# Kernel tuning notes

Hardware: AMD Instinct MI355X
Metric: run time of the kernel (lower is better)

Reference implementation:

```python
import jax, jax.numpy as jnp
import numpy as np

N_NODES = 100000
N_EDGES = 1600000
N_GRAPHS = 512
IN_C, HID, OUT_C = 128, 128, 64


def gcn_conv(x, W, b, src, dst, num_nodes):
    # PyG GCNConv: add self-loops, symmetric normalization D^-1/2 (A+I) D^-1/2, then linear.
    h = x @ W  # [N, F_out]
    deg = jnp.ones((num_nodes,), h.dtype).at[dst].add(jnp.ones((src.shape[0],), h.dtype))  # +1 for self-loop
    dinv = jax.lax.rsqrt(deg)
    norm = dinv[src] * dinv[dst]  # [E]
    agg = jnp.zeros_like(h).at[dst].add(h[src] * norm[:, None])
    agg = agg + h * (dinv * dinv)[:, None]  # self-loop contribution
    return agg + b


def global_mean_pool(x, batch, num_graphs):
    s = jax.ops.segment_sum(x, batch, num_segments=num_graphs)
    cnt = jax.ops.segment_sum(jnp.ones((x.shape[0],), x.dtype), batch, num_segments=num_graphs)
    return s / jnp.maximum(cnt, 1.0)[:, None]


def setup_inputs() -> dict:
    key = jax.random.key(0)
    ks = jax.random.split(key, 16)
    glorot = lambda k, i, o: jax.random.normal(k, (i, o), jnp.float32) * (2.0 / (i + o)) ** 0.5
    inp = {
        "x": jax.random.normal(ks[0], (N_NODES, IN_C), jnp.float32),
        "edge_index": jax.random.randint(ks[1], (2, N_EDGES), 0, N_NODES, jnp.int64 if jax.config.jax_enable_x64 else jnp.int32),
        "batch": jnp.sort(jax.random.randint(ks[2], (N_NODES,), 0, N_GRAPHS)),
        "W1": glorot(ks[3], IN_C, HID), "b1": jnp.zeros((HID,), jnp.float32),
        "W2": glorot(ks[4], HID, HID), "b2": jnp.zeros((HID,), jnp.float32),
        "W3": glorot(ks[5], HID, HID), "b3": jnp.zeros((HID,), jnp.float32),
        "Wf1": glorot(ks[6], HID, HID * 4), "bf1": jnp.zeros((HID * 4,), jnp.float32),
        "Wf2": glorot(ks[7], HID * 4, HID * 2), "bf2": jnp.zeros((HID * 2,), jnp.float32),
        "Wf3": glorot(ks[8], HID * 2, HID), "bf3": jnp.zeros((HID,), jnp.float32),
        "Wf4": glorot(ks[9], HID, OUT_C), "bf4": jnp.zeros((OUT_C,), jnp.float32),
    }
    return inp


def reference(x, edge_index, batch, W1, b1, W2, b2, W3, b3,
              Wf1, bf1, Wf2, bf2, Wf3, bf3, Wf4, bf4):
    src, dst = edge_index[0], edge_index[1]
    h = jax.nn.relu(gcn_conv(x, W1, b1, src, dst, N_NODES))
    h = jax.nn.relu(gcn_conv(h, W2, b2, src, dst, N_NODES))
    h = gcn_conv(h, W3, b3, src, dst, N_NODES)
    f = global_mean_pool(h, batch, N_GRAPHS)  # [G, HID]
    z = jax.nn.relu(f @ Wf1 + bf1)
    z = jax.nn.relu(z @ Wf2 + bf2)
    z = jax.nn.relu(z @ Wf3 + bf3)
    z = z @ Wf4 + bf4
    return (f, z)
```

## Files before the change

kernel.cpp:

```cpp
#include <hip/hip_runtime.h>
#include <hip/hip_bf16.h>

#define NN 100000
#define NE 1600000
#define NG 512
#define HID 128
#define PPART 391
#define EPB 4096
#define CAP 4608

typedef __attribute__((ext_vector_type(8))) short short8;
typedef __attribute__((ext_vector_type(4))) float floatx4;

__device__ inline ushort f2bf(float f) {
  uint u = __float_as_uint(f);
  u += 0x7fff + ((u >> 16) & 1);
  return (ushort)(u >> 16);
}
__device__ inline uint pack2(float lo, float hi) {
  return (uint)f2bf(lo) | ((uint)f2bf(hi) << 16);
}
__device__ inline float bflo(uint u) { return __uint_as_float(u << 16); }
__device__ inline float bfhi(uint u) { return __uint_as_float(u & 0xffff0000u); }

__global__ void k_pinit(int* __restrict__ pcur) {
  int p = blockIdx.x * 256 + threadIdx.x;
  if (p < PPART) pcur[p] = p * CAP;
}

__global__ __launch_bounds__(256) void k_part(const int* __restrict__ src,
                                              const int* __restrict__ dst,
                                              int* __restrict__ pcur,
                                              uint* __restrict__ pedge) {
  __shared__ int hist[PPART];
  __shared__ int base[PPART];
  int t = threadIdx.x;
  for (int i = t; i < PPART; i += 256) hist[i] = 0;
  __syncthreads();
  int e0 = blockIdx.x * EPB;
  int d_[16];
#pragma unroll
  for (int l = 0; l < 16; ++l) {
    int e = e0 + l * 256 + t;
    if (e < NE) {
      int d = dst[e];
      d_[l] = d;
      atomicAdd(&hist[d >> 8], 1);
    } else {
      d_[l] = -1;
    }
  }
  __syncthreads();
  for (int i = t; i < PPART; i += 256) {
    int h = hist[i];
    base[i] = h ? atomicAdd(&pcur[i], h) : 0;
  }
  __syncthreads();
#pragma unroll
  for (int l = 0; l < 16; ++l) {
    int e = e0 + l * 256 + t;
    if (e < NE) {
      int d = d_[l];
      int s = src[e];
      int pos = atomicAdd(&base[d >> 8], 1);
      pedge[pos] = (uint)s | ((uint)(d & 255) << 24);
    }
  }
}

__global__ __launch_bounds__(512) void k_pscan(const int* __restrict__ pcur,
                                               int* __restrict__ pbase) {
  __shared__ int ws[8];
  int t = threadIdx.x, lane = t & 63, wid = t >> 6;
  int v = (t < PPART) ? (pcur[t] - t * CAP) : 0;
  int iv = v;
  for (int o = 1; o < 64; o <<= 1) {
    int n = __shfl_up(iv, o, 64);
    if (lane >= o) iv += n;
  }
  if (lane == 63) ws[wid] = iv;
  __syncthreads();
  int add = 0;
#pragma unroll
  for (int w = 0; w < 8; ++w) add += (w < wid) ? ws[w] : 0;
  if (t < PPART) pbase[t] = iv - v + add;
  if (t == 0) {
    int tot = 0;
#pragma unroll
    for (int w = 0; w < 8; ++w) tot += ws[w];
    pbase[PPART] = tot;
  }
}

__global__ __launch_bounds__(256) void k_cnt2(const int* __restrict__ pbase,
                                              const uint* __restrict__ pedge,
                                              int* __restrict__ offsets,
                                              float* __restrict__ dinv) {
  __shared__ int cnt_s[256];
  __shared__ int ws[4];
  int p = blockIdx.x;
  int n0 = p << 8;
  int t = threadIdx.x;
  int lim = NN - n0; if (lim > 256) lim = 256;
  int size = pbase[p + 1] - pbase[p];
  int s = p * CAP;
  cnt_s[t] = 0;
  __syncthreads();
  for (int i = s + t; i < s + size; i += 256) atomicAdd(&cnt_s[pedge[i] >> 24], 1);
  __syncthreads();
  int v = cnt_s[t];
  int lane = t & 63, wid = t >> 6;
  int iv = v;
  for (int o = 1; o < 64; o <<= 1) {
    int n = __shfl_up(iv, o, 64);
    if (lane >= o) iv += n;
  }
  if (lane == 63) ws[wid] = iv;
  __syncthreads();
  int add = 0;
#pragma unroll
  for (int w = 0; w < 4; ++w) add += (w < wid) ? ws[w] : 0;
  int excl = iv - v + add;
  if (t < lim) {
    offsets[n0 + t] = pbase[p] + excl;
    dinv[n0 + t] = 1.0f / sqrtf((float)(v + 1));
  }
  if (p == PPART - 1 && t == 0) offsets[NN] = NE;
}

__global__ __launch_bounds__(256) void k_place(const int* __restrict__ pbase,
                                               const uint* __restrict__ pedge,
                                               const int* __restrict__ offsets,
                                               const float* __restrict__ dinv,
                                               int2* __restrict__ emeta) {
  __shared__ int cur[256];
  int p = blockIdx.x;
  int n0 = p << 8;
  int t = threadIdx.x;
  int lim = NN - n0; if (lim > 256) lim = 256;
  if (t < lim) cur[t] = offsets[n0 + t];
  __syncthreads();
  int size = pbase[p + 1] - pbase[p];
  int s = p * CAP;
  for (int i = s + t; i < s + size; i += 256) {
    uint pv = pedge[i];
    int srcn = (int)(pv & 0xFFFFFFu);
    int pos = atomicAdd(&cur[pv >> 24], 1);
    int2 m;
    m.x = srcn;
    m.y = __float_as_int(dinv[srcn]);
    emeta[pos] = m;
  }
}

__global__ __launch_bounds__(128) void k_prepW(const float* __restrict__ W,
                                               ushort* __restrict__ wt) {
  int c = blockIdx.x;
  int r = threadIdx.x;
  float v = W[r * 128 + c];
  wt[c * 128 + (((r >> 3) ^ (c & 15)) << 3) + (r & 7)] = f2bf(v);
}

__global__ __launch_bounds__(256) void k_gemm(const ushort* __restrict__ Xb,
                                              const ushort* __restrict__ wt,
                                              ushort* __restrict__ Hb) {
  __shared__ ushort sW[128 * 128];
  int t = threadIdx.x;
#pragma unroll
  for (int l = 0; l < 8; ++l) {
    int idx = t + l * 256;
    ((uint4*)sW)[idx] = ((const uint4*)wt)[idx];
  }
  __syncthreads();
  int wid = t >> 6, lane = t & 63;
  int row0 = blockIdx.x * 64 + wid * 16;
  int arow = row0 + (lane & 15);
  if (arow >= NN) arow = NN - 1;
  const ushort* aptr = Xb + (size_t)arow * 128 + ((lane >> 4) * 8);
  floatx4 acc[8];
#pragma unroll
  for (int n = 0; n < 8; ++n) acc[n] = (floatx4)(0.f);
#pragma unroll
  for (int kb = 0; kb < 4; ++kb) {
    short8 a = *(const short8*)(aptr + kb * 32);
    int kslot = kb * 4 + (lane >> 4);
#pragma unroll
    for (int n = 0; n < 8; ++n) {
      int col = n * 16 + (lane & 15);
      const ushort* bp = sW + col * 128 + ((kslot ^ (col & 15)) << 3);
      short8 b = *(const short8*)bp;
      acc[n] = __builtin_amdgcn_mfma_f32_16x16x32_bf16(a, b, acc[n], 0, 0, 0);
    }
  }
  int srow_base = row0 + (lane >> 4) * 4;
#pragma unroll
  for (int r = 0; r < 4; ++r) {
    int grow = srow_base + r;
    if (grow < NN) {
      ushort* out = Hb + (size_t)grow * 128 + (lane & 15);
#pragma unroll
      for (int n = 0; n < 8; ++n) out[n * 16] = f2bf(acc[n][r]);
    }
  }
}

__global__ __launch_bounds__(256) void k_gemmf(const float* __restrict__ Xf,
                                               const ushort* __restrict__ wt,
                                               ushort* __restrict__ Hb) {
  __shared__ ushort sW[128 * 128];
  int t = threadIdx.x;
#pragma unroll
  for (int l = 0; l < 8; ++l) {
    int idx = t + l * 256;
    ((uint4*)sW)[idx] = ((const uint4*)wt)[idx];
  }
  __syncthreads();
  int wid = t >> 6, lane = t & 63;
  int row0 = blockIdx.x * 64 + wid * 16;
  int arow = row0 + (lane & 15);
  if (arow >= NN) arow = NN - 1;
  const float* aptr = Xf + (size_t)arow * 128 + ((lane >> 4) * 8);
  floatx4 acc[8];
#pragma unroll
  for (int n = 0; n < 8; ++n) acc[n] = (floatx4)(0.f);
#pragma unroll
  for (int kb = 0; kb < 4; ++kb) {
    float4 f0 = *(const float4*)(aptr + kb * 32);
    float4 f1 = *(const float4*)(aptr + kb * 32 + 4);
    union { uint4 u; short8 s; } av;
    av.u.x = pack2(f0.x, f0.y);
    av.u.y = pack2(f0.z, f0.w);
    av.u.z = pack2(f1.x, f1.y);
    av.u.w = pack2(f1.z, f1.w);
    short8 a = av.s;
    int kslot = kb * 4 + (lane >> 4);
#pragma unroll
    for (int n = 0; n < 8; ++n) {
      int col = n * 16 + (lane & 15);
      const ushort* bp = sW + col * 128 + ((kslot ^ (col & 15)) << 3);
      short8 b = *(const short8*)bp;
      acc[n] = __builtin_amdgcn_mfma_f32_16x16x32_bf16(a, b, acc[n], 0, 0, 0);
    }
  }
  int srow_base = row0 + (lane >> 4) * 4;
#pragma unroll
  for (int r = 0; r < 4; ++r) {
    int grow = srow_base + r;
    if (grow < NN) {
      ushort* out = Hb + (size_t)grow * 128 + (lane & 15);
#pragma unroll
      for (int n = 0; n < 8; ++n) out[n * 16] = f2bf(acc[n][r]);
    }
  }
}

__global__ __launch_bounds__(256) void k_agg(const ushort* __restrict__ H,
                                             const float* __restrict__ bias,
                                             const float* __restrict__ dinv,
                                             const int* __restrict__ offsets,
                                             const int2* __restrict__ emeta,
                                             ushort* __restrict__ Hout, int do_relu) {
  int node = blockIdx.x * 16 + (threadIdx.x >> 4);
  if (node >= NN) return;
  int lane = threadIdx.x & 63;
  int c8 = lane & 15;
  int gbase = lane & 48;
  float di = dinv[node];
  int s = offsets[node], e = offsets[node + 1];
  float acc[8];
#pragma unroll
  for (int j = 0; j < 8; ++j) acc[j] = 0.f;
  for (int i = s; i < e; i += 16) {
    int idx = i + c8;
    bool vld = idx < e;
    int2 m = emeta[vld ? idx : s];
    int msrc = m.x;
    float mw = vld ? __int_as_float(m.y) : 0.0f;
#pragma unroll
    for (int half = 0; half < 2; ++half) {
      int sxu[8];
      float wu[8];
#pragma unroll
      for (int u = 0; u < 8; ++u) {
        int sl = gbase + half * 8 + u;
        sxu[u] = __shfl(msrc, sl, 64);
        wu[u] = __shfl(mw, sl, 64);
      }
      uint4 vx[8];
#pragma unroll
      for (int u = 0; u < 8; ++u)
        vx[u] = *((const uint4*)(H + (size_t)sxu[u] * 128) + c8);
#pragma unroll
      for (int u = 0; u < 8; ++u) {
        acc[0] += bflo(vx[u].x) * wu[u];
        acc[1] += bfhi(vx[u].x) * wu[u];
        acc[2] += bflo(vx[u].y) * wu[u];
        acc[3] += bfhi(vx[u].y) * wu[u];
        acc[4] += bflo(vx[u].z) * wu[u];
        acc[5] += bfhi(vx[u].z) * wu[u];
        acc[6] += bflo(vx[u].w) * wu[u];
        acc[7] += bfhi(vx[u].w) * wu[u];
      }
    }
  }
  uint4 hv = *((const uint4*)(H + (size_t)node * 128) + c8);
  float hb[8] = {bflo(hv.x), bfhi(hv.x), bflo(hv.y), bfhi(hv.y),
                 bflo(hv.z), bfhi(hv.z), bflo(hv.w), bfhi(hv.w)};
  float dii = di * di;
  const float* bp = bias + c8 * 8;
  float r[8];
#pragma unroll
  for (int j = 0; j < 8; ++j) {
    float vv = acc[j] * di + hb[j] * dii + bp[j];
    if (do_relu) vv = fmaxf(vv, 0.f);
    r[j] = vv;
  }
  uint4 o;
  o.x = pack2(r[0], r[1]);
  o.y = pack2(r[2], r[3]);
  o.z = pack2(r[4], r[5]);
  o.w = pack2(r[6], r[7]);
  *((uint4*)(Hout + (size_t)node * 128) + c8) = o;
}

__device__ inline int lower_bound(const int* a, int n, int v) {
  int lo = 0, hi = n;
  while (lo < hi) {
    int m = (lo + hi) >> 1;
    if (a[m] < v) lo = m + 1; else hi = m;
  }
  return lo;
}

__global__ __launch_bounds__(128) void k_pool(const ushort* __restrict__ H,
                                              const int* __restrict__ batch,
                                              float* __restrict__ f) {
  int g = blockIdx.x;
  int c = threadIdx.x;
  int s = lower_bound(batch, NN, g);
  int e = lower_bound(batch, NN, g + 1);
  float acc = 0.f;
#pragma unroll 4
  for (int i = s; i < e; ++i)
    acc += __uint_as_float(((uint)H[(size_t)i * 128 + c]) << 16);
  f[g * 128 + c] = acc / fmaxf((float)(e - s), 1.0f);
}

__global__ __launch_bounds__(256) void k_mgemm(const float* __restrict__ X,
                                               const float* __restrict__ W,
                                               const float* __restrict__ bias,
                                               float* __restrict__ Y,
                                               int M, int K, int N, int do_relu) {
  __shared__ float sA[32][32];
  __shared__ float sB[32][64];
  int t = threadIdx.x;
  int tn = t & 15, tm = t >> 4;
  int m0 = blockIdx.y * 32;
  int n0 = blockIdx.x * 64;
  float acc[2][4];
#pragma unroll
  for (int i = 0; i < 2; ++i)
#pragma unroll
    for (int j = 0; j < 4; ++j) acc[i][j] = 0.f;

  for (int kb = 0; kb < K; kb += 32) {
    {
      int r = t >> 3, kq = t & 7;
      float4 v = *(const float4*)(X + (size_t)(m0 + r) * K + kb + kq * 4);
      sA[kq * 4 + 0][r] = v.x;
      sA[kq * 4 + 1][r] = v.y;
      sA[kq * 4 + 2][r] = v.z;
      sA[kq * 4 + 3][r] = v.w;
    }
#pragma unroll
    for (int l = 0; l < 2; ++l) {
      int idx = t * 2 + l;
      int kr = idx >> 4, nq = idx & 15;
      *(float4*)&sB[kr][nq * 4] = *(const float4*)(W + (size_t)(kb + kr) * N + n0 + nq * 4);
    }
    __syncthreads();
#pragma unroll
    for (int k = 0; k < 32; ++k) {
      float a[2], b[4];
      a[0] = sA[k][tm * 2];
      a[1] = sA[k][tm * 2 + 1];
      *(float4*)b = *(float4*)&sB[k][tn * 4];
#pragma unroll
      for (int i = 0; i < 2; ++i)
#pragma unroll
        for (int j = 0; j < 4; ++j) acc[i][j] += a[i] * b[j];
    }
    __syncthreads();
  }
  float4 bv = *(const float4*)(bias + n0 + tn * 4);
#pragma unroll
  for (int i = 0; i < 2; ++i) {
    float4 o;
    o.x = acc[i][0] + bv.x;
    o.y = acc[i][1] + bv.y;
    o.z = acc[i][2] + bv.z;
    o.w = acc[i][3] + bv.w;
    if (do_relu) {
      o.x = fmaxf(o.x, 0.f);
      o.y = fmaxf(o.y, 0.f);
      o.z = fmaxf(o.z, 0.f);
      o.w = fmaxf(o.w, 0.f);
    }
    *(float4*)(Y + (size_t)(m0 + tm * 2 + i) * N + n0 + tn * 4) = o;
  }
}

extern "C" void kernel_launch(void* const* d_in, const int* in_sizes, int n_in,
                              void* d_out, int out_size, void* d_ws, size_t ws_size,
                              hipStream_t stream) {
  const float* x    = (const float*)d_in[0];
  const int* ei     = (const int*)d_in[1];
  const int* batch  = (const int*)d_in[2];
  const float* W1   = (const float*)d_in[3];  const float* b1  = (const float*)d_in[4];
  const float* W2   = (const float*)d_in[5];  const float* b2  = (const float*)d_in[6];
  const float* W3   = (const float*)d_in[7];  const float* b3  = (const float*)d_in[8];
  const float* Wf1  = (const float*)d_in[9];  const float* bf1 = (const float*)d_in[10];
  const float* Wf2  = (const float*)d_in[11]; const float* bf2 = (const float*)d_in[12];
  const float* Wf3  = (const float*)d_in[13]; const float* bf3 = (const float*)d_in[14];
  const float* Wf4  = (const float*)d_in[15]; const float* bf4 = (const float*)d_in[16];
  const int* src = ei;
  const int* dst = ei + NE;

  char* ws = (char*)d_ws;
  size_t off = 0;
  auto alloc = [&](size_t bytes) {
    void* p = ws + off;
    off += (bytes + 255) & ~(size_t)255;
    return p;
  };
  ushort* B0     = (ushort*)alloc((size_t)NN * 128 * 2);
  ushort* B1     = (ushort*)alloc((size_t)NN * 128 * 2);
  ushort* B2     = (ushort*)alloc((size_t)NN * 128 * 2);
  float* dinv    = (float*)alloc((size_t)NN * 4);
  int*   offsets = (int*)alloc((size_t)(NN + 1) * 4);
  uint*  pedge   = (uint*)alloc((size_t)PPART * CAP * 4);
  int2*  emeta   = (int2*)alloc((size_t)NE * 8);
  int*   pbase   = (int*)alloc((size_t)(PPART + 1) * 4);
  int*   pcur    = (int*)alloc((size_t)PPART * 4);
  ushort* wt1    = (ushort*)alloc(128 * 128 * 2);
  ushort* wt2    = (ushort*)alloc(128 * 128 * 2);
  ushort* wt3    = (ushort*)alloc(128 * 128 * 2);
  float* t1      = (float*)alloc((size_t)NG * 512 * 4);
  float* t2      = (float*)alloc((size_t)NG * 256 * 4);
  float* t3      = (float*)alloc((size_t)NG * 128 * 4);

  float* f_out = (float*)d_out;
  float* z_out = (float*)d_out + NG * HID;

  k_pinit<<<(PPART + 255) / 256, 256, 0, stream>>>(pcur);
  k_part<<<(NE + EPB - 1) / EPB, 256, 0, stream>>>(src, dst, pcur, pedge);
  k_pscan<<<1, 512, 0, stream>>>(pcur, pbase);
  k_cnt2<<<PPART, 256, 0, stream>>>(pbase, pedge, offsets, dinv);
  k_place<<<PPART, 256, 0, stream>>>(pbase, pedge, offsets, dinv, emeta);

  k_prepW<<<128, 128, 0, stream>>>(W1, wt1);
  k_prepW<<<128, 128, 0, stream>>>(W2, wt2);
  k_prepW<<<128, 128, 0, stream>>>(W3, wt3);

  int gemm_grid = (NN + 63) / 64;
  int agg_grid = (NN + 15) / 16;

  k_gemmf<<<gemm_grid, 256, 0, stream>>>(x, wt1, B1);
  k_agg<<<agg_grid, 256, 0, stream>>>(B1, b1, dinv, offsets, emeta, B2, 1);
  k_gemm<<<gemm_grid, 256, 0, stream>>>(B2, wt2, B1);
  k_agg<<<agg_grid, 256, 0, stream>>>(B1, b2, dinv, offsets, emeta, B0, 1);
  k_gemm<<<gemm_grid, 256, 0, stream>>>(B0, wt3, B1);
  k_agg<<<agg_grid, 256, 0, stream>>>(B1, b3, dinv, offsets, emeta, B2, 0);

  k_pool<<<NG, 128, 0, stream>>>(B2, batch, f_out);

  k_mgemm<<<dim3(8, 16), 256, 0, stream>>>(f_out, Wf1, bf1, t1, NG, 128, 512, 1);
  k_mgemm<<<dim3(4, 16), 256, 0, stream>>>(t1, Wf2, bf2, t2, NG, 512, 256, 1);
  k_mgemm<<<dim3(2, 16), 256, 0, stream>>>(t2, Wf3, bf3, t3, NG, 256, 128, 1);
  k_mgemm<<<dim3(1, 16), 256, 0, stream>>>(t3, Wf4, bf4, z_out, NG, 128, 64, 0);
}
```

Measured before the change: 367.2 us.

## Shrink edge metadata to src-only, fuse setup kernels, widen pool loads

Edge metadata is cut from int2 (src plus dinv[src]) to a plain src index, and the aggregation kernel instead gathers dinv[src] per edge. This halves the edge-list storage and traffic in the placement kernel at the cost of an extra random 4-byte gather per edge in each of the three aggregations. The three weight-prep kernels and the partition-cursor init are fused into one launch. Separately, the partition kernel loads src alongside dst in its first pass, and the pooling kernel reads bf16 pairs as 32-bit words split over two row halves.

```diff
diff --git a/kernel.cpp b/kernel.cpp
--- a/kernel.cpp
+++ b/kernel.cpp
@@ -23,9 +23,26 @@
 __device__ inline float bflo(uint u) { return __uint_as_float(u << 16); }
 __device__ inline float bfhi(uint u) { return __uint_as_float(u & 0xffff0000u); }
 
-__global__ void k_pinit(int* __restrict__ pcur) {
-  int p = blockIdx.x * 256 + threadIdx.x;
-  if (p < PPART) pcur[p] = p * CAP;
+__global__ __launch_bounds__(128) void k_setup(const float* __restrict__ W1,
+                                               const float* __restrict__ W2,
+                                               const float* __restrict__ W3,
+                                               ushort* __restrict__ wt1,
+                                               ushort* __restrict__ wt2,
+                                               ushort* __restrict__ wt3,
+                                               int* __restrict__ pcur) {
+  int b = blockIdx.x;
+  int r = threadIdx.x;
+  if (b < 384) {
+    int w = b >> 7;
+    int c = b & 127;
+    const float* W = (w == 0) ? W1 : ((w == 1) ? W2 : W3);
+    ushort* wt = (w == 0) ? wt1 : ((w == 1) ? wt2 : wt3);
+    float v = W[r * 128 + c];
+    wt[c * 128 + (((r >> 3) ^ (c & 15)) << 3) + (r & 7)] = f2bf(v);
+  } else {
+    int p = (b - 384) * 128 + r;
+    if (p < PPART) pcur[p] = p * CAP;
+  }
 }
 
 __global__ __launch_bounds__(256) void k_part(const int* __restrict__ src,
@@ -38,12 +55,13 @@
   for (int i = t; i < PPART; i += 256) hist[i] = 0;
   __syncthreads();
   int e0 = blockIdx.x * EPB;
-  int d_[16];
+  int d_[16], s_[16];
 #pragma unroll
   for (int l = 0; l < 16; ++l) {
     int e = e0 + l * 256 + t;
     if (e < NE) {
       int d = dst[e];
+      s_[l] = src[e];
       d_[l] = d;
       atomicAdd(&hist[d >> 8], 1);
     } else {
@@ -58,12 +76,10 @@
   __syncthreads();
 #pragma unroll
   for (int l = 0; l < 16; ++l) {
-    int e = e0 + l * 256 + t;
-    if (e < NE) {
+    if (d_[l] >= 0) {
       int d = d_[l];
-      int s = src[e];
       int pos = atomicAdd(&base[d >> 8], 1);
-      pedge[pos] = (uint)s | ((uint)(d & 255) << 24);
+      pedge[pos] = (uint)s_[l] | ((uint)(d & 255) << 24);
     }
   }
 }
@@ -131,8 +147,7 @@
 __global__ __launch_bounds__(256) void k_place(const int* __restrict__ pbase,
                                                const uint* __restrict__ pedge,
                                                const int* __restrict__ offsets,
-                                               const float* __restrict__ dinv,
-                                               int2* __restrict__ emeta) {
+                                               int* __restrict__ srcs) {
   __shared__ int cur[256];
   int p = blockIdx.x;
   int n0 = p << 8;
@@ -144,21 +159,9 @@
   int s = p * CAP;
   for (int i = s + t; i < s + size; i += 256) {
     uint pv = pedge[i];
-    int srcn = (int)(pv & 0xFFFFFFu);
     int pos = atomicAdd(&cur[pv >> 24], 1);
-    int2 m;
-    m.x = srcn;
-    m.y = __float_as_int(dinv[srcn]);
-    emeta[pos] = m;
-  }
-}
-
-__global__ __launch_bounds__(128) void k_prepW(const float* __restrict__ W,
-                                               ushort* __restrict__ wt) {
-  int c = blockIdx.x;
-  int r = threadIdx.x;
-  float v = W[r * 128 + c];
-  wt[c * 128 + (((r >> 3) ^ (c & 15)) << 3) + (r & 7)] = f2bf(v);
+    srcs[pos] = (int)(pv & 0xFFFFFFu);
+  }
 }
 
 __global__ __launch_bounds__(256) void k_gemm(const ushort* __restrict__ Xb,
@@ -258,7 +261,7 @@
                                              const float* __restrict__ bias,
                                              const float* __restrict__ dinv,
                                              const int* __restrict__ offsets,
-                                             const int2* __restrict__ emeta,
+                                             const int* __restrict__ srcs,
                                              ushort* __restrict__ Hout, int do_relu) {
   int node = blockIdx.x * 16 + (threadIdx.x >> 4);
   if (node >= NN) return;
@@ -273,9 +276,8 @@
   for (int i = s; i < e; i += 16) {
     int idx = i + c8;
     bool vld = idx < e;
-    int2 m = emeta[vld ? idx : s];
-    int msrc = m.x;
-    float mw = vld ? __int_as_float(m.y) : 0.0f;
+    int msrc = srcs[vld ? idx : s];
+    float mv = vld ? 1.0f : 0.0f;
 #pragma unroll
     for (int half = 0; half < 2; ++half) {
       int sxu[8];
@@ -284,8 +286,10 @@
       for (int u = 0; u < 8; ++u) {
         int sl = gbase + half * 8 + u;
         sxu[u] = __shfl(msrc, sl, 64);
-        wu[u] = __shfl(mw, sl, 64);
+        wu[u] = __shfl(mv, sl, 64);
       }
+#pragma unroll
+      for (int u = 0; u < 8; ++u) wu[u] *= dinv[sxu[u]];
       uint4 vx[8];
 #pragma unroll
       for (int u = 0; u < 8; ++u)
@@ -335,15 +339,25 @@
 __global__ __launch_bounds__(128) void k_pool(const ushort* __restrict__ H,
                                               const int* __restrict__ batch,
                                               float* __restrict__ f) {
+  __shared__ float part[128][2];
   int g = blockIdx.x;
-  int c = threadIdx.x;
+  int t = threadIdx.x;
   int s = lower_bound(batch, NN, g);
   int e = lower_bound(batch, NN, g + 1);
-  float acc = 0.f;
-#pragma unroll 4
-  for (int i = s; i < e; ++i)
-    acc += __uint_as_float(((uint)H[(size_t)i * 128 + c]) << 16);
-  f[g * 128 + c] = acc / fmaxf((float)(e - s), 1.0f);
+  int half = t >> 6;
+  int cu = t & 63;
+  float a0 = 0.f, a1 = 0.f;
+  const uint* H32 = (const uint*)H;
+  for (int i = s + half; i < e; i += 2) {
+    uint u = H32[(size_t)i * 64 + cu];
+    a0 += bflo(u);
+    a1 += bfhi(u);
+  }
+  part[2 * cu + 0][half] = a0;
+  part[2 * cu + 1][half] = a1;
+  __syncthreads();
+  float tot = part[t][0] + part[t][1];
+  f[g * 128 + t] = tot / fmaxf((float)(e - s), 1.0f);
 }
 
 __global__ __launch_bounds__(256) void k_mgemm(const float* __restrict__ X,
@@ -439,7 +453,7 @@
   float* dinv    = (float*)alloc((size_t)NN * 4);
   int*   offsets = (int*)alloc((size_t)(NN + 1) * 4);
   uint*  pedge   = (uint*)alloc((size_t)PPART * CAP * 4);
-  int2*  emeta   = (int2*)alloc((size_t)NE * 8);
+  int*   srcs    = (int*)alloc((size_t)NE * 4);
   int*   pbase   = (int*)alloc((size_t)(PPART + 1) * 4);
   int*   pcur    = (int*)alloc((size_t)PPART * 4);
   ushort* wt1    = (ushort*)alloc(128 * 128 * 2);
@@ -452,25 +466,21 @@
   float* f_out = (float*)d_out;
   float* z_out = (float*)d_out + NG * HID;
 
-  k_pinit<<<(PPART + 255) / 256, 256, 0, stream>>>(pcur);
+  k_setup<<<384 + (PPART + 127) / 128, 128, 0, stream>>>(W1, W2, W3, wt1, wt2, wt3, pcur);
   k_part<<<(NE + EPB - 1) / EPB, 256, 0, stream>>>(src, dst, pcur, pedge);
   k_pscan<<<1, 512, 0, stream>>>(pcur, pbase);
   k_cnt2<<<PPART, 256, 0, stream>>>(pbase, pedge, offsets, dinv);
-  k_place<<<PPART, 256, 0, stream>>>(pbase, pedge, offsets, dinv, emeta);
-
-  k_prepW<<<128, 128, 0, stream>>>(W1, wt1);
-  k_prepW<<<128, 128, 0, stream>>>(W2, wt2);
-  k_prepW<<<128, 128, 0, stream>>>(W3, wt3);
+  k_place<<<PPART, 256, 0, stream>>>(pbase, pedge, offsets, srcs);
 
   int gemm_grid = (NN + 63) / 64;
   int agg_grid = (NN + 15) / 16;
 
   k_gemmf<<<gemm_grid, 256, 0, stream>>>(x, wt1, B1);
-  k_agg<<<agg_grid, 256, 0, stream>>>(B1, b1, dinv, offsets, emeta, B2, 1);
+  k_agg<<<agg_grid, 256, 0, stream>>>(B1, b1, dinv, offsets, srcs, B2, 1);
   k_gemm<<<gemm_grid, 256, 0, stream>>>(B2, wt2, B1);
-  k_agg<<<agg_grid, 256, 0, stream>>>(B1, b2, dinv, offsets, emeta, B0, 1);
+  k_agg<<<agg_grid, 256, 0, stream>>>(B1, b2, dinv, offsets, srcs, B0, 1);
   k_gemm<<<gemm_grid, 256, 0, stream>>>(B0, wt3, B1);
-  k_agg<<<agg_grid, 256, 0, stream>>>(B1, b3, dinv, offsets, emeta, B2, 0);
+  k_agg<<<agg_grid, 256, 0, stream>>>(B1, b3, dinv, offsets, srcs, B2, 0);
 
   k_pool<<<NG, 128, 0, stream>>>(B2, batch, f_out);
 
```

Measured after the change: 415.5 us. 13.1% more time.
